# Kernel tuning notes

Hardware: AMD Instinct MI355X
Metric: run time of the kernel (lower is better)

## Reference

```python
import jax, jax.numpy as jnp
import numpy as np

H, NH, QLORA, KVLORA, DN, DR, DV = 2048, 16, 1536, 512, 128, 64, 128
QD = DN + DR  # 192
EPS = 1e-6
ROPE_BASE = 10000.0


def rmsnorm(x, g):
    var = jnp.mean(x * x, axis=-1, keepdims=True)
    return x * jax.lax.rsqrt(var + EPS) * g


def rotate_half(x):
    x1, x2 = jnp.split(x, 2, axis=-1)
    return jnp.concatenate([-x2, x1], axis=-1)


def rope_cos_sin(seq_len):
    inv_freq = 1.0 / (ROPE_BASE ** (jnp.arange(0, DR, 2, dtype=jnp.float32) / DR))
    t = jnp.arange(seq_len, dtype=jnp.float32)
    freqs = jnp.outer(t, inv_freq)           # [S, DR/2]
    emb = jnp.concatenate([freqs, freqs], -1)  # [S, DR]
    return jnp.cos(emb), jnp.sin(emb)


def setup_inputs() -> dict:
    key = jax.random.key(0)
    ks = jax.random.split(key, 6)
    B, S = 2, 2048
    sc = 0.02
    return {
        "hidden_states": jax.random.normal(ks[0], (B, S, H), jnp.float32),
        "w_qa": jax.random.normal(ks[1], (QLORA, H), jnp.float32) * sc,
        "g_qa": jnp.ones((QLORA,), jnp.float32),
        "w_qb": jax.random.normal(ks[2], (NH * QD, QLORA), jnp.float32) * sc,
        "w_kva": jax.random.normal(ks[3], (KVLORA + DR, H), jnp.float32) * sc,
        "g_kva": jnp.ones((KVLORA,), jnp.float32),
        "w_kvb": jax.random.normal(ks[4], (NH * (DN + DV), KVLORA), jnp.float32) * sc,
        "w_o": jax.random.normal(ks[5], (H, NH * DV), jnp.float32) * sc,
    }


def reference(hidden_states, w_qa, g_qa, w_qb, w_kva, g_kva, w_kvb, w_o):
    B, S, _ = hidden_states.shape
    # Q path: low-rank down-proj -> RMSNorm -> up-proj
    q_a = hidden_states @ w_qa.T                        # [B,S,QLORA]
    q = rmsnorm(q_a, g_qa) @ w_qb.T                     # [B,S,NH*QD]
    q = q.reshape(B, S, NH, QD).transpose(0, 2, 1, 3)   # [B,NH,S,QD]
    q_nope, q_pe = q[..., :DN], q[..., DN:]
    # KV path: joint down-proj with MQA rope slice
    ckv = hidden_states @ w_kva.T                       # [B,S,KVLORA+DR]
    compressed_kv, k_pe = ckv[..., :KVLORA], ckv[..., KVLORA:]
    k_pe = k_pe.reshape(B, S, 1, DR).transpose(0, 2, 1, 3)  # [B,1,S,DR]
    kv = rmsnorm(compressed_kv, g_kva) @ w_kvb.T        # [B,S,NH*(DN+DV)]
    kv = kv.reshape(B, S, NH, DN + DV).transpose(0, 2, 1, 3)
    k_nope, v = kv[..., :DN], kv[..., DN:]              # [B,NH,S,DN], [B,NH,S,DV]
    # decoupled RoPE on rope sub-dims only
    cos, sin = rope_cos_sin(S)                          # [S,DR]
    cos = cos[None, None]; sin = sin[None, None]
    q_pe = q_pe * cos + rotate_half(q_pe) * sin
    k_pe = k_pe * cos + rotate_half(k_pe) * sin
    query = jnp.concatenate([q_nope, q_pe], -1)         # [B,NH,S,QD]
    key = jnp.concatenate([k_nope, jnp.broadcast_to(k_pe, (B, NH, S, DR))], -1)
    # causal SDPA with scale = QD**-0.5
    scale = QD ** (-0.5)
    scores = jnp.einsum("bhsd,bhtd->bhst", query, key) * scale
    mask = jnp.tril(jnp.ones((S, S), bool))
    scores = jnp.where(mask, scores, jnp.finfo(scores.dtype).min)
    attn = jax.nn.softmax(scores, axis=-1)
    out = jnp.einsum("bhst,bhtd->bhsd", attn, v)        # [B,NH,S,DV]
    out = out.transpose(0, 2, 1, 3).reshape(B, S, NH * DV)
    return out @ w_o.T
```

## Files before the change

### kernel.cpp

```cpp
#include <hip/hip_runtime.h>
#include <cstdint>
#include <cstring>

typedef short short8 __attribute__((ext_vector_type(8)));
typedef float float4v __attribute__((ext_vector_type(4)));
typedef float float4g __attribute__((ext_vector_type(4)));
typedef unsigned short ushort4v __attribute__((ext_vector_type(4)));
typedef unsigned int uint2v __attribute__((ext_vector_type(2)));

typedef __attribute__((address_space(3))) unsigned int lds_uint;
typedef __attribute__((address_space(1))) const unsigned int glob_uint;

static __device__ __forceinline__ void async16(void* lds, const void* g) {
    __builtin_amdgcn_global_load_lds((glob_uint*)g, (lds_uint*)lds, 16, 0, 0);
}

static __device__ __forceinline__ float b2f(unsigned short u) {
    unsigned int x = ((unsigned int)u) << 16;
    float f;
    __builtin_memcpy(&f, &x, 4);
    return f;
}
static __device__ __forceinline__ unsigned short f2b(float f) {
    unsigned int x;
    __builtin_memcpy(&x, &f, 4);
    unsigned int r = (x + 0x7fffu + ((x >> 16) & 1u)) >> 16;
    return (unsigned short)r;
}

__global__ __launch_bounds__(256) void k_f2b6(
    const float* __restrict__ s0, unsigned short* __restrict__ d0,
    const float* __restrict__ s1, unsigned short* __restrict__ d1,
    const float* __restrict__ s2, unsigned short* __restrict__ d2,
    const float* __restrict__ s3, unsigned short* __restrict__ d3,
    const float* __restrict__ s4, unsigned short* __restrict__ d4,
    const float* __restrict__ s5, unsigned short* __restrict__ d5,
    float qs) {
    int blk = blockIdx.x;
    const float* s; unsigned short* d; float sc = 1.f; int rel;
    if (blk < 8192)       { s = s0; d = d0; rel = blk; }
    else if (blk < 11264) { s = s1; d = d1; rel = blk - 8192; }
    else if (blk < 15872) { s = s2; d = d2; rel = blk - 11264; sc = qs; }
    else if (blk < 17024) { s = s3; d = d3; rel = blk - 15872; }
    else if (blk < 19072) { s = s4; d = d4; rel = blk - 17024; }
    else                  { s = s5; d = d5; rel = blk - 19072; }
    int i = (rel * 256 + threadIdx.x) * 4;
    float4g v = *(const float4g*)(s + i);
    ushort4v r;
    r.x = f2b(v.x * sc); r.y = f2b(v.y * sc); r.z = f2b(v.z * sc); r.w = f2b(v.w * sc);
    *(ushort4v*)(d + i) = r;
}

static __device__ __forceinline__ void gemm_bt_body(
    const unsigned short* __restrict__ A, int lda,
    const unsigned short* __restrict__ W,
    void* __restrict__ C, int ldc,
    int N, int K, int c_fp32, int bx, int by) {
    __shared__ __align__(16) unsigned short As[128 * 32];
    __shared__ __align__(16) unsigned short Ws[128 * 32];
    const int tid = threadIdx.x;
    const int m0 = by * 128, n0 = bx * 128;
    const int wave = tid >> 6, lane = tid & 63;
    const int wm = (wave >> 1) * 64, wn = (wave & 1) * 64;
    const int lrow = lane & 15, quad = lane >> 4;
    const int srow = lane >> 2, spiece = lane & 3;

    float4v acc[4][4];
    float4v z = {0.f, 0.f, 0.f, 0.f};
#pragma unroll
    for (int i = 0; i < 4; i++)
#pragma unroll
        for (int j = 0; j < 4; j++) acc[i][j] = z;

    for (int k0 = 0; k0 < K; k0 += 32) {
#pragma unroll
        for (int ii = 0; ii < 2; ++ii) {
            int i = wave + ii * 4;
            int row = i * 16 + srow;
            async16(&As[i * 512], &A[(size_t)(m0 + row) * lda + k0 + spiece * 8]);
            int wr = n0 + row;
            if (wr > N - 1) wr = N - 1;
            async16(&Ws[i * 512], &W[(size_t)wr * K + k0 + spiece * 8]);
        }
        __syncthreads();
        short8 af[4], bfr[4];
#pragma unroll
        for (int i = 0; i < 4; i++)
            af[i] = *(const short8*)&As[(wm + i * 16 + lrow) * 32 + quad * 8];
#pragma unroll
        for (int i = 0; i < 4; i++)
            bfr[i] = *(const short8*)&Ws[(wn + i * 16 + lrow) * 32 + quad * 8];
#pragma unroll
        for (int i = 0; i < 4; i++)
#pragma unroll
            for (int j = 0; j < 4; j++)
                acc[i][j] = __builtin_amdgcn_mfma_f32_16x16x32_bf16(af[i], bfr[j], acc[i][j], 0, 0, 0);
        __syncthreads();
    }

    const int rbase = quad * 4;
#pragma unroll
    for (int i = 0; i < 4; i++) {
#pragma unroll
        for (int j = 0; j < 4; j++) {
            int col = n0 + wn + j * 16 + lrow;
            if (col >= N) continue;
#pragma unroll
            for (int r = 0; r < 4; r++) {
                int row = m0 + wm + i * 16 + rbase + r;
                float v = acc[i][j][r];
                if (c_fp32)
                    ((float*)C)[(size_t)row * ldc + col] = v;
                else
                    ((unsigned short*)C)[(size_t)row * ldc + col] = f2b(v);
            }
        }
    }
}

__global__ __launch_bounds__(256, 3)
void k_gemm_bt(const unsigned short* __restrict__ A, int lda,
               const unsigned short* __restrict__ W,
               void* __restrict__ C, int ldc,
               int N, int K, int c_fp32) {
    gemm_bt_body(A, lda, W, C, ldc, N, K, c_fp32, blockIdx.x, blockIdx.y);
}

__global__ __launch_bounds__(256, 3)
void k_gemm_dual(const unsigned short* __restrict__ A0, int lda0,
                 const unsigned short* __restrict__ W0, void* __restrict__ C0,
                 int ldc0, int N0, int K0, int nbx0,
                 const unsigned short* __restrict__ A1, int lda1,
                 const unsigned short* __restrict__ W1, void* __restrict__ C1,
                 int ldc1, int N1, int K1) {
    int bx = blockIdx.x;
    if (bx < nbx0) {
        gemm_bt_body(A0, lda0, W0, C0, ldc0, N0, K0, 0, bx, blockIdx.y);
    } else {
        gemm_bt_body(A1, lda1, W1, C1, ldc1, N1, K1, 0, bx - nbx0, blockIdx.y);
    }
}

__global__ __launch_bounds__(192) void k_norm2(
    unsigned short* __restrict__ qa, const float* __restrict__ g_qa,
    unsigned short* __restrict__ ckv, const float* __restrict__ g_kva) {
    __shared__ float wsum[3];
    int blk = blockIdx.x;
    int tid = threadIdx.x;
    if (blk < 4096) {
        size_t base = (size_t)blk * 1536 + tid * 8;
        short8 v8 = *(const short8*)(qa + base);
        float vf[8];
        float ss = 0.f;
#pragma unroll
        for (int i = 0; i < 8; i++) {
            vf[i] = b2f((unsigned short)v8[i]);
            ss += vf[i] * vf[i];
        }
        for (int off = 32; off > 0; off >>= 1) ss += __shfl_xor(ss, off);
        int wave = tid >> 6, lane = tid & 63;
        if (lane == 0) wsum[wave] = ss;
        __syncthreads();
        ss = wsum[0] + wsum[1] + wsum[2];
        float scale = rsqrtf(ss * (1.f / 1536.f) + 1e-6f);
        short8 r8;
#pragma unroll
        for (int i = 0; i < 8; i++) r8[i] = (short)f2b(vf[i] * scale * g_qa[tid * 8 + i]);
        *(short8*)(qa + base) = r8;
    } else {
        int row = blk - 4096;
        if (tid < 64) {
            size_t base = (size_t)row * 576 + tid * 8;
            short8 v8 = *(const short8*)(ckv + base);
            float vf[8];
            float ss = 0.f;
#pragma unroll
            for (int i = 0; i < 8; i++) {
                vf[i] = b2f((unsigned short)v8[i]);
                ss += vf[i] * vf[i];
            }
            for (int off = 32; off > 0; off >>= 1) ss += __shfl_xor(ss, off);
            float scale = rsqrtf(ss * (1.f / 512.f) + 1e-6f);
            short8 r8;
#pragma unroll
            for (int i = 0; i < 8; i++) r8[i] = (short)f2b(vf[i] * scale * g_kva[tid * 8 + i]);
            *(short8*)(ckv + base) = r8;
        } else if (tid < 96) {
            int d = tid - 64;
            int s = row & 2047;
            size_t base = (size_t)row * 576 + 512;
            float inv = exp2f((float)d * -0.4152410118609203f);
            float f = (float)s * inv;
            float c, sn;
            sincosf(f, &sn, &c);
            float x1 = b2f(ckv[base + d]), x2 = b2f(ckv[base + d + 32]);
            ckv[base + d] = f2b(x1 * c - x2 * sn);
            ckv[base + d + 32] = f2b(x2 * c + x1 * sn);
        }
    }
}

__global__ __launch_bounds__(256) void k_transpose_v(const unsigned short* __restrict__ kv,
                                                     unsigned short* __restrict__ vt) {
    int bh = blockIdx.z;
    int b = bh >> 4, h = bh & 15;
    int s0 = blockIdx.x * 32, d0 = blockIdx.y * 32;
    __shared__ unsigned short t[32][33];
    int tx = threadIdx.x & 31, ty = threadIdx.x >> 5;
#pragma unroll
    for (int i = 0; i < 4; i++) {
        int s = s0 + ty + i * 8;
        t[ty + i * 8][tx] = kv[(size_t)(b * 2048 + s) * 4096 + h * 256 + 128 + d0 + tx];
    }
    __syncthreads();
#pragma unroll
    for (int i = 0; i < 4; i++) {
        int d = d0 + ty + i * 8;
        vt[((size_t)bh * 128 + d) * 2048 + s0 + tx] = t[tx][ty + i * 8];
    }
}

__global__ __launch_bounds__(256, 2)
void k_attn9(const unsigned short* __restrict__ q,
             const unsigned short* __restrict__ kv,
             const unsigned short* __restrict__ ckv,
             const unsigned short* __restrict__ vt,
             unsigned short* __restrict__ ao)
{
    __shared__ __align__(16) unsigned short Ks[2][12288];
    __shared__ __align__(16) unsigned short Vs[8192];
    __shared__ __align__(16) unsigned short Pl[4][1280];

    const int lb = blockIdx.x;
    const int qt = (lb < 256) ? (lb >> 5) : 15 - ((lb & 255) >> 5);
    const int bh = lb & 31;
    const int b = bh >> 4, h = bh & 15;
    const int tid = threadIdx.x, wave = tid >> 6, lane = tid & 63;
    const int lrow = lane & 15, quad = lane >> 4;
    const int srow = lane >> 2, spiece = lane & 3;
    const int tok0 = b * 2048 + qt * 128;
    unsigned short* Pw = Pl[wave];

    const int colx = spiece ^ ((srow >> 1) & 3);
    const int qx = (quad ^ ((lrow >> 1) & 3)) * 8;

    short8 qf[2][6];
#pragma unroll
    for (int mi = 0; mi < 2; mi++) {
        int row = wave * 32 + mi * 16 + lrow;
        const unsigned short* qp = q + (size_t)(tok0 + row) * 3072 + h * 192;
#pragma unroll
        for (int ks = 0; ks < 6; ks++) qf[mi][ks] = *(const short8*)(qp + ks * 32 + quad * 8);
        float sp = (float)(qt * 128 + row);
#pragma unroll
        for (int j = 0; j < 8; j++) {
            float inv = exp2f((float)(quad * 8 + j) * -0.4152410118609203f);
            float f = sp * inv;
            float c, sn;
            sincosf(f, &sn, &c);
            float x1 = b2f((unsigned short)qf[mi][4][j]);
            float x2 = b2f((unsigned short)qf[mi][5][j]);
            qf[mi][4][j] = (short)f2b(x1 * c - x2 * sn);
            qf[mi][5][j] = (short)f2b(x2 * c + x1 * sn);
        }
    }

    short8 ones;
#pragma unroll
    for (int j = 0; j < 8; j++) ones[j] = (short)0x3F80;

    float m_st[2];
    m_st[0] = m_st[1] = -__builtin_inff();
    float4v z4 = {0.f, 0.f, 0.f, 0.f};
    float4v o[2][8], osum[2];
#pragma unroll
    for (int mi = 0; mi < 2; mi++) {
        osum[mi] = z4;
#pragma unroll
        for (int dt = 0; dt < 8; dt++) o[mi][dt] = z4;
    }

    const int nk = 2 * qt + 2;

    auto stageK = [&](int kt, int buf) {
        const int kb = kt * 64;
#pragma unroll
        for (int ii = 0; ii < 6; ++ii) {
            int id = wave * 6 + ii;
            int ks = id >> 2;
            int row = (id & 3) * 16 + srow;
            int key = b * 2048 + kb + row;
            const unsigned short* g =
                (ks < 4) ? kv + (size_t)key * 4096 + h * 256 + ks * 32 + colx * 8
                         : ckv + (size_t)key * 576 + 512 + (ks - 4) * 32 + colx * 8;
            async16(&Ks[buf][id * 512], g);
        }
    };
    auto stageV = [&](int kt) {
        const int kb = kt * 64;
#pragma unroll
        for (int ii = 0; ii < 4; ++ii) {
            int id = wave * 4 + ii;
            int d = (id & 7) * 16 + srow;
            const unsigned short* g =
                vt + ((size_t)bh * 128 + d) * 2048 + kb + (id >> 3) * 32 + colx * 8;
            async16(&Vs[id * 512], g);
        }
    };

    stageK(0, 0);

    for (int kt = 0; kt < nk; ++kt) {
        __syncthreads();
        stageV(kt);
        if (kt + 1 < nk) stageK(kt + 1, (kt + 1) & 1);
        const unsigned short* Kb = Ks[kt & 1];
        const int kb = kt * 64;

        float4v sc[2][4];
#pragma unroll
        for (int mi = 0; mi < 2; mi++)
#pragma unroll
            for (int nt = 0; nt < 4; nt++) sc[mi][nt] = z4;
        __builtin_amdgcn_s_setprio(1);
#pragma unroll
        for (int ks = 0; ks < 6; ks++) {
#pragma unroll
            for (int nt = 0; nt < 4; nt++) {
                short8 kf = *(const short8*)&Kb[ks * 2048 + nt * 512 + lrow * 32 + qx];
                sc[0][nt] = __builtin_amdgcn_mfma_f32_16x16x32_bf16(kf, qf[0][ks], sc[0][nt], 0, 0, 0);
                sc[1][nt] = __builtin_amdgcn_mfma_f32_16x16x32_bf16(kf, qf[1][ks], sc[1][nt], 0, 0, 0);
            }
        }
        __builtin_amdgcn_s_setprio(0);

        if (kt >= nk - 2) {
#pragma unroll
            for (int mi = 0; mi < 2; mi++) {
                int rowc = qt * 128 + wave * 32 + mi * 16 + lrow;
#pragma unroll
                for (int nt = 0; nt < 4; nt++)
#pragma unroll
                    for (int r = 0; r < 4; r++) {
                        int keyc = kb + nt * 16 + quad * 4 + r;
                        if (keyc > rowc) sc[mi][nt][r] = -__builtin_inff();
                    }
            }
        }

        float mx[2];
#pragma unroll
        for (int mi = 0; mi < 2; mi++) {
            float m = sc[mi][0][0];
#pragma unroll
            for (int nt = 0; nt < 4; nt++)
#pragma unroll
                for (int r = 0; r < 4; r++) m = fmaxf(m, sc[mi][nt][r]);
            m = fmaxf(m, __shfl_xor(m, 16));
            m = fmaxf(m, __shfl_xor(m, 32));
            mx[mi] = m;
        }
        bool within = (mx[0] <= m_st[0] + 6.f) && (mx[1] <= m_st[1] + 6.f);
        if (!__all(within)) {
            float alpha[2];
#pragma unroll
            for (int mi = 0; mi < 2; mi++) {
                float mnew = fmaxf(m_st[mi], mx[mi]);
                alpha[mi] = exp2f(m_st[mi] - mnew);
                m_st[mi] = mnew;
            }
            float arow[2][4];
#pragma unroll
            for (int mi = 0; mi < 2; mi++)
#pragma unroll
                for (int r = 0; r < 4; r++) arow[mi][r] = __shfl(alpha[mi], quad * 4 + r);
#pragma unroll
            for (int mi = 0; mi < 2; mi++) {
#pragma unroll
                for (int r = 0; r < 4; r++) osum[mi][r] *= arow[mi][r];
#pragma unroll
                for (int dt = 0; dt < 8; dt++)
#pragma unroll
                    for (int r = 0; r < 4; r++) o[mi][dt][r] *= arow[mi][r];
            }
        }
        uint2v pk[2][4];
#pragma unroll
        for (int mi = 0; mi < 2; mi++) {
#pragma unroll
            for (int nt = 0; nt < 4; nt++) {
                float p0 = exp2f(sc[mi][nt][0] - m_st[mi]);
                float p1 = exp2f(sc[mi][nt][1] - m_st[mi]);
                float p2 = exp2f(sc[mi][nt][2] - m_st[mi]);
                float p3 = exp2f(sc[mi][nt][3] - m_st[mi]);
                pk[mi][nt].x = (unsigned int)f2b(p0) | ((unsigned int)f2b(p1) << 16);
                pk[mi][nt].y = (unsigned int)f2b(p2) | ((unsigned int)f2b(p3) << 16);
            }
        }

        __syncthreads();

#pragma unroll
        for (int ks2 = 0; ks2 < 2; ks2++) {
#pragma unroll
            for (int mi = 0; mi < 2; mi++) {
                int row = mi * 16 + lrow;
                *(uint2v*)&Pw[row * 40 + quad * 4] = pk[mi][ks2 * 2];
                *(uint2v*)&Pw[row * 40 + 16 + quad * 4] = pk[mi][ks2 * 2 + 1];
            }
            short8 pa0 = *(const short8*)&Pw[lrow * 40 + quad * 8];
            short8 pa1 = *(const short8*)&Pw[(16 + lrow) * 40 + quad * 8];
            __builtin_amdgcn_s_setprio(1);
#pragma unroll
            for (int dt = 0; dt < 8; dt++) {
                short8 vf = *(const short8*)&Vs[(ks2 * 8 + dt) * 512 + lrow * 32 + qx];
                o[0][dt] = __builtin_amdgcn_mfma_f32_16x16x32_bf16(pa0, vf, o[0][dt], 0, 0, 0);
                o[1][dt] = __builtin_amdgcn_mfma_f32_16x16x32_bf16(pa1, vf, o[1][dt], 0, 0, 0);
            }
            osum[0] = __builtin_amdgcn_mfma_f32_16x16x32_bf16(pa0, ones, osum[0], 0, 0, 0);
            osum[1] = __builtin_amdgcn_mfma_f32_16x16x32_bf16(pa1, ones, osum[1], 0, 0, 0);
            __builtin_amdgcn_s_setprio(0);
        }
    }

#pragma unroll
    for (int mi = 0; mi < 2; mi++) {
#pragma unroll
        for (int r = 0; r < 4; r++) {
            float linv = 1.f / osum[mi][r];
            unsigned short* dst =
                ao + (size_t)(tok0 + wave * 32 + mi * 16 + quad * 4 + r) * 2048 + h * 128;
#pragma unroll
            for (int dt = 0; dt < 8; dt++) dst[dt * 16 + lrow] = f2b(o[mi][dt][r] * linv);
        }
    }
}

extern "C" void kernel_launch(void* const* d_in, const int* in_sizes, int n_in,
                              void* d_out, int out_size, void* d_ws, size_t ws_size,
                              hipStream_t stream) {
    (void)in_sizes; (void)n_in; (void)out_size; (void)ws_size;
    const float* hs    = (const float*)d_in[0];
    const float* w_qa  = (const float*)d_in[1];
    const float* g_qa  = (const float*)d_in[2];
    const float* w_qb  = (const float*)d_in[3];
    const float* w_kva = (const float*)d_in[4];
    const float* g_kva = (const float*)d_in[5];
    const float* w_kvb = (const float*)d_in[6];
    const float* w_o   = (const float*)d_in[7];

    char* ws = (char*)d_ws;
    size_t off = 0;
    auto alloc = [&](size_t bytes) -> unsigned short* {
        unsigned short* p = (unsigned short*)(ws + off);
        off += (bytes + 255) & ~(size_t)255;
        return p;
    };
    unsigned short* hb    = alloc(4096ull * 2048 * 2);
    unsigned short* wqa   = alloc(1536ull * 2048 * 2);
    unsigned short* wqb   = alloc(3072ull * 1536 * 2);
    unsigned short* wkva  = alloc(576ull * 2048 * 2);
    unsigned short* wkvb  = alloc(4096ull * 512 * 2);
    unsigned short* wo    = alloc(2048ull * 2048 * 2);
    unsigned short* qa    = alloc(4096ull * 1536 * 2);
    unsigned short* ckv   = alloc(4096ull * 576 * 2);
    unsigned short* qbuf  = alloc(4096ull * 3072 * 2);
    unsigned short* kvbuf = alloc(4096ull * 4096 * 2);
    unsigned short* vtb   = alloc(32ull * 128 * 2048 * 2);
    unsigned short* ao    = alloc(4096ull * 2048 * 2);

    const float qscale = 0.07216878364870323f * 1.4426950408889634f;

    k_f2b6<<<dim3(23168), dim3(256), 0, stream>>>(
        hs, hb, w_qa, wqa, w_qb, wqb, w_kva, wkva, w_kvb, wkvb, w_o, wo, qscale);

    k_gemm_dual<<<dim3(17, 32), 256, 0, stream>>>(
        hb, 2048, wqa, qa, 1536, 1536, 2048, 12,
        hb, 2048, wkva, ckv, 576, 576, 2048);

    k_norm2<<<dim3(8192), dim3(192), 0, stream>>>(qa, g_qa, ckv, g_kva);

    k_gemm_dual<<<dim3(56, 32), 256, 0, stream>>>(
        qa, 1536, wqb, qbuf, 3072, 3072, 1536, 24,
        ckv, 576, wkvb, kvbuf, 4096, 4096, 512);

    k_transpose_v<<<dim3(64, 4, 32), 256, 0, stream>>>(kvbuf, vtb);
    k_attn9<<<dim3(512), 256, 0, stream>>>(qbuf, kvbuf, ckv, vtb, ao);
    k_gemm_bt<<<dim3(16, 32), 256, 0, stream>>>(ao, 2048, wo, d_out, 2048, 2048, 2048, 1);
}
```

Baseline: 431.9 us.

## Fuse V transpose into kv GEMM epilogue and reorder attention tiles heavy-first

The kv up-projection GEMM now writes the V half directly in transposed [b,h,d,s] layout through a new epilogue mode, which removes the separate transpose kernel and one launch. The attention kernel's block-to-query-tile mapping is changed so the longest causal tiles are scheduled first, for better tail balance. The fused epilogue uses scattered 2-byte stores with a large stride, which may coalesce poorly.

```diff
diff --git a/kernel.cpp b/kernel.cpp
--- a/kernel.cpp
+++ b/kernel.cpp
@@ -55,7 +55,8 @@
     const unsigned short* __restrict__ A, int lda,
     const unsigned short* __restrict__ W,
     void* __restrict__ C, int ldc,
-    int N, int K, int c_fp32, int bx, int by) {
+    int N, int K, int mode, int bx, int by,
+    unsigned short* __restrict__ VT) {
     __shared__ __align__(16) unsigned short As[128 * 32];
     __shared__ __align__(16) unsigned short Ws[128 * 32];
     const int tid = threadIdx.x;
@@ -105,14 +106,29 @@
         for (int j = 0; j < 4; j++) {
             int col = n0 + wn + j * 16 + lrow;
             if (col >= N) continue;
-#pragma unroll
-            for (int r = 0; r < 4; r++) {
-                int row = m0 + wm + i * 16 + rbase + r;
-                float v = acc[i][j][r];
-                if (c_fp32)
-                    ((float*)C)[(size_t)row * ldc + col] = v;
-                else
-                    ((unsigned short*)C)[(size_t)row * ldc + col] = f2b(v);
+            if (mode == 2) {
+                int dd = col & 255, h = col >> 8;
+#pragma unroll
+                for (int r = 0; r < 4; r++) {
+                    int row = m0 + wm + i * 16 + rbase + r;
+                    float v = acc[i][j][r];
+                    if (dd < 128) {
+                        ((unsigned short*)C)[(size_t)row * ldc + col] = f2b(v);
+                    } else {
+                        int b = row >> 11, s = row & 2047;
+                        VT[((size_t)(b * 16 + h) * 128 + (dd - 128)) * 2048 + s] = f2b(v);
+                    }
+                }
+            } else {
+#pragma unroll
+                for (int r = 0; r < 4; r++) {
+                    int row = m0 + wm + i * 16 + rbase + r;
+                    float v = acc[i][j][r];
+                    if (mode == 1)
+                        ((float*)C)[(size_t)row * ldc + col] = v;
+                    else
+                        ((unsigned short*)C)[(size_t)row * ldc + col] = f2b(v);
+                }
             }
         }
     }
@@ -122,8 +138,8 @@
 void k_gemm_bt(const unsigned short* __restrict__ A, int lda,
                const unsigned short* __restrict__ W,
                void* __restrict__ C, int ldc,
-               int N, int K, int c_fp32) {
-    gemm_bt_body(A, lda, W, C, ldc, N, K, c_fp32, blockIdx.x, blockIdx.y);
+               int N, int K, int mode) {
+    gemm_bt_body(A, lda, W, C, ldc, N, K, mode, blockIdx.x, blockIdx.y, nullptr);
 }
 
 __global__ __launch_bounds__(256, 3)
@@ -132,12 +148,13 @@
                  int ldc0, int N0, int K0, int nbx0,
                  const unsigned short* __restrict__ A1, int lda1,
                  const unsigned short* __restrict__ W1, void* __restrict__ C1,
-                 int ldc1, int N1, int K1) {
+                 int ldc1, int N1, int K1, int mode1,
+                 unsigned short* __restrict__ VT) {
     int bx = blockIdx.x;
     if (bx < nbx0) {
-        gemm_bt_body(A0, lda0, W0, C0, ldc0, N0, K0, 0, bx, blockIdx.y);
+        gemm_bt_body(A0, lda0, W0, C0, ldc0, N0, K0, 0, bx, blockIdx.y, nullptr);
     } else {
-        gemm_bt_body(A1, lda1, W1, C1, ldc1, N1, K1, 0, bx - nbx0, blockIdx.y);
+        gemm_bt_body(A1, lda1, W1, C1, ldc1, N1, K1, mode1, bx - nbx0, blockIdx.y, VT);
     }
 }
 
@@ -200,39 +217,19 @@
     }
 }
 
-__global__ __launch_bounds__(256) void k_transpose_v(const unsigned short* __restrict__ kv,
-                                                     unsigned short* __restrict__ vt) {
-    int bh = blockIdx.z;
-    int b = bh >> 4, h = bh & 15;
-    int s0 = blockIdx.x * 32, d0 = blockIdx.y * 32;
-    __shared__ unsigned short t[32][33];
-    int tx = threadIdx.x & 31, ty = threadIdx.x >> 5;
-#pragma unroll
-    for (int i = 0; i < 4; i++) {
-        int s = s0 + ty + i * 8;
-        t[ty + i * 8][tx] = kv[(size_t)(b * 2048 + s) * 4096 + h * 256 + 128 + d0 + tx];
-    }
-    __syncthreads();
-#pragma unroll
-    for (int i = 0; i < 4; i++) {
-        int d = d0 + ty + i * 8;
-        vt[((size_t)bh * 128 + d) * 2048 + s0 + tx] = t[tx][ty + i * 8];
-    }
-}
-
 __global__ __launch_bounds__(256, 2)
-void k_attn9(const unsigned short* __restrict__ q,
-             const unsigned short* __restrict__ kv,
-             const unsigned short* __restrict__ ckv,
-             const unsigned short* __restrict__ vt,
-             unsigned short* __restrict__ ao)
+void k_attn10(const unsigned short* __restrict__ q,
+              const unsigned short* __restrict__ kv,
+              const unsigned short* __restrict__ ckv,
+              const unsigned short* __restrict__ vt,
+              unsigned short* __restrict__ ao)
 {
     __shared__ __align__(16) unsigned short Ks[2][12288];
     __shared__ __align__(16) unsigned short Vs[8192];
     __shared__ __align__(16) unsigned short Pl[4][1280];
 
     const int lb = blockIdx.x;
-    const int qt = (lb < 256) ? (lb >> 5) : 15 - ((lb & 255) >> 5);
+    const int qt = (lb < 256) ? (15 - (lb >> 5)) : ((lb & 255) >> 5);
     const int bh = lb & 31;
     const int b = bh >> 4, h = bh & 15;
     const int tid = threadIdx.x, wave = tid >> 6, lane = tid & 63;
@@ -476,15 +473,14 @@
 
     k_gemm_dual<<<dim3(17, 32), 256, 0, stream>>>(
         hb, 2048, wqa, qa, 1536, 1536, 2048, 12,
-        hb, 2048, wkva, ckv, 576, 576, 2048);
+        hb, 2048, wkva, ckv, 576, 576, 2048, 0, nullptr);
 
     k_norm2<<<dim3(8192), dim3(192), 0, stream>>>(qa, g_qa, ckv, g_kva);
 
     k_gemm_dual<<<dim3(56, 32), 256, 0, stream>>>(
         qa, 1536, wqb, qbuf, 3072, 3072, 1536, 24,
-        ckv, 576, wkvb, kvbuf, 4096, 4096, 512);
-
-    k_transpose_v<<<dim3(64, 4, 32), 256, 0, stream>>>(kvbuf, vtb);
-    k_attn9<<<dim3(512), 256, 0, stream>>>(qbuf, kvbuf, ckv, vtb, ao);
+        ckv, 576, wkvb, kvbuf, 4096, 4096, 512, 2, vtb);
+
+    k_attn10<<<dim3(512), 256, 0, stream>>>(qbuf, kvbuf, ckv, vtb, ao);
     k_gemm_bt<<<dim3(16, 32), 256, 0, stream>>>(ao, 2048, wo, d_out, 2048, 2048, 2048, 1);
 }
```

Measured after the change: 464.5 us. +7.6%, slower.
